# Optimization experiments

Measured on AMD Instinct MI355X. Metric: run time of the kernel, lower is better.

Reference implementation:

```python
import jax, jax.numpy as jnp
import numpy as np

HIDDEN = 2048
HEADS = 16
HEAD_DIM = HIDDEN // HEADS

def setup_inputs() -> dict:
    key = jax.random.key(0)
    ks = jax.random.split(key, 9)
    B, S = 1, 4096
    scale = 1.0 / np.sqrt(HIDDEN)
    x = jax.random.normal(ks[0], (B, S, HIDDEN), dtype=jnp.float32)
    Wq = jax.random.normal(ks[1], (HIDDEN, HIDDEN), dtype=jnp.float32) * scale
    Wk = jax.random.normal(ks[2], (HIDDEN, HIDDEN), dtype=jnp.float32) * scale
    Wv = jax.random.normal(ks[3], (HIDDEN, HIDDEN), dtype=jnp.float32) * scale
    Wo = jax.random.normal(ks[4], (HIDDEN, HIDDEN), dtype=jnp.float32) * scale
    bq = jax.random.normal(ks[5], (HIDDEN,), dtype=jnp.float32) * 0.01
    bk = jax.random.normal(ks[6], (HIDDEN,), dtype=jnp.float32) * 0.01
    bv = jax.random.normal(ks[7], (HIDDEN,), dtype=jnp.float32) * 0.01
    bo = jax.random.normal(ks[8], (HIDDEN,), dtype=jnp.float32) * 0.01
    return {"x": x, "Wq": Wq, "bq": bq, "Wk": Wk, "bk": bk, "Wv": Wv, "bv": bv, "Wo": Wo, "bo": bo}

def reference(x, Wq, bq, Wk, bk, Wv, bv, Wo, bo):
    B, S, D = x.shape
    H, Hd = HEADS, HEAD_DIM
    # projections (nn.Linear: x @ W^T + b)
    Q = (x @ Wq.T + bq).reshape(B, S, H, Hd).transpose(0, 2, 1, 3)  # [B,H,S,Hd]
    K = (x @ Wk.T + bk).reshape(B, S, H, Hd).transpose(0, 2, 1, 3)
    V = (x @ Wv.T + bv).reshape(B, S, H, Hd).transpose(0, 2, 1, 3)
    scores = jnp.einsum('bhqd,bhkd->bhqk', Q, K) / jnp.sqrt(jnp.float32(Hd))
    attn = jax.nn.softmax(scores, axis=-1)
    out = jnp.einsum('bhqk,bhkd->bhqd', attn, V)  # [B,H,S,Hd]
    out = out.transpose(0, 2, 1, 3).reshape(B, S, D)
    return out @ Wo.T + bo
```

## Files before the change

kernel.cpp:

```cpp
#include <hip/hip_runtime.h>

#define S_LEN  4096
#define DMODEL 2048
#define NHEADS 16
#define HDIM   128

typedef __bf16 bf16x8 __attribute__((ext_vector_type(8)));
typedef __bf16 bf16x2 __attribute__((ext_vector_type(2)));
typedef float  f32x4  __attribute__((ext_vector_type(4)));
typedef float  f32x16 __attribute__((ext_vector_type(16)));

__device__ __forceinline__ unsigned short f2b(float f) {
    unsigned int u = __float_as_uint(f);
    unsigned int r = (u + 0x7fffu + ((u >> 16) & 1u)) >> 16;
    return (unsigned short)r;
}

__device__ __forceinline__ unsigned int pkbf16(float a, float b) {
#if __has_builtin(__builtin_amdgcn_cvt_pk_bf16_f32)
    bf16x2 t = __builtin_amdgcn_cvt_pk_bf16_f32(a, b);
    return *(unsigned int*)&t;
#else
    return (unsigned int)f2b(a) | ((unsigned int)f2b(b) << 16);
#endif
}

__device__ __forceinline__ f32x4 mfma16(bf16x8 a, bf16x8 b, f32x4 c) {
    return __builtin_amdgcn_mfma_f32_16x16x32_bf16(a, b, c, 0, 0, 0);
}

__device__ __forceinline__ f32x16 mfma32(bf16x8 a, bf16x8 b, f32x16 c) {
    return __builtin_amdgcn_mfma_f32_32x32x16_bf16(a, b, c, 0, 0, 0);
}

__device__ __forceinline__ void ldg2lds16(const void* g, void* l) {
    __builtin_amdgcn_global_load_lds(
        (__attribute__((address_space(1))) void*)(void*)g,
        (__attribute__((address_space(3))) void*)l, 16, 0, 0);
}

__global__ __launch_bounds__(256) void cvt_bf16(
    const float* __restrict__ src, unsigned short* __restrict__ dst, int n4)
{
    int i = blockIdx.x * blockDim.x + threadIdx.x;
    if (i < n4) {
        float4 v = ((const float4*)src)[i];
        uint2 h;
        h.x = pkbf16(v.x, v.y); h.y = pkbf16(v.z, v.w);
        ((uint2*)dst)[i] = h;
    }
}

__global__ __launch_bounds__(256) void cvt_bf16_w4(
    const float* __restrict__ w0, const float* __restrict__ w1,
    const float* __restrict__ w2, const float* __restrict__ w3,
    unsigned short* __restrict__ d0, unsigned short* __restrict__ d1,
    unsigned short* __restrict__ d2, unsigned short* __restrict__ d3)
{
    const int z = blockIdx.y;
    const float* src = (z == 0) ? w0 : (z == 1) ? w1 : (z == 2) ? w2 : w3;
    unsigned short* dst = (z == 0) ? d0 : (z == 1) ? d1 : (z == 2) ? d2 : d3;
    int i = blockIdx.x * blockDim.x + threadIdx.x;
    float4 v = ((const float4*)src)[i];
    uint2 h;
    h.x = pkbf16(v.x, v.y); h.y = pkbf16(v.z, v.w);
    ((uint2*)dst)[i] = h;
}

__global__ __launch_bounds__(256, 2) void gemm_qkv(
    const unsigned short* __restrict__ xb,
    const unsigned short* __restrict__ Wqb, const float* __restrict__ bq,
    const unsigned short* __restrict__ Wkb, const float* __restrict__ bk,
    const unsigned short* __restrict__ Wvb, const float* __restrict__ bv,
    unsigned short* __restrict__ Qb, unsigned short* __restrict__ Kb,
    unsigned short* __restrict__ Vb)
{
    const int id  = blockIdx.x + 16 * (blockIdx.y + 32 * blockIdx.z);
    const int swz = (id & 7) * 192 + (id >> 3);
    const int n0 = (swz & 15) * 128;
    const int m0 = ((swz >> 4) & 31) * 128;
    const int z  = swz >> 9;

    const unsigned short* B = (z == 0) ? Wqb : (z == 1) ? Wkb : Wvb;
    const float* bias        = (z == 0) ? bq  : (z == 1) ? bk  : bv;
    unsigned short* C        = (z == 0) ? Qb  : (z == 1) ? Kb  : Vb;
    const float oscale = (z == 0) ? 0.12751743f : 1.0f;

    __shared__ alignas(16) unsigned short As[128 * 32];
    __shared__ alignas(16) unsigned short Bs[128 * 32];

    const int tid = threadIdx.x;
    const int w = tid >> 6, lane = tid & 63, lo = lane & 15, qd = lane >> 4;
    const int wm = (w >> 1) * 64, wn = (w & 1) * 64;
    const int rsel = lane >> 2, csel = (lane & 3) * 8;

    f32x4 acc[4][4] = {};

    for (int k0 = 0; k0 < DMODEL; k0 += 32) {
#pragma unroll
        for (int i = 0; i < 2; i++) {
            int c = w * 2 + i;
            ldg2lds16(&xb[(size_t)(m0 + c * 16 + rsel) * DMODEL + k0 + csel],
                      &As[c * 512]);
            ldg2lds16(&B [(size_t)(n0 + c * 16 + rsel) * DMODEL + k0 + csel],
                      &Bs[c * 512]);
        }
        __syncthreads();

        bf16x8 af[4], bfr[4];
#pragma unroll
        for (int i = 0; i < 4; i++)
            af[i] = *(const bf16x8*)&As[(wm + i * 16 + lo) * 32 + qd * 8];
#pragma unroll
        for (int j = 0; j < 4; j++)
            bfr[j] = *(const bf16x8*)&Bs[(wn + j * 16 + lo) * 32 + qd * 8];
#pragma unroll
        for (int i = 0; i < 4; i++)
#pragma unroll
            for (int j = 0; j < 4; j++)
                acc[i][j] = mfma16(af[i], bfr[j], acc[i][j]);
        __syncthreads();
    }

#pragma unroll
    for (int j = 0; j < 4; j++) {
        int n = n0 + wn + j * 16 + lo;
        float bv_ = bias[n];
#pragma unroll
        for (int i = 0; i < 4; i++) {
#pragma unroll
            for (int r = 0; r < 4; r++) {
                int m = m0 + wm + i * 16 + qd * 4 + r;
                C[(size_t)m * DMODEL + n] = f2b((acc[i][j][r] + bv_) * oscale);
            }
        }
    }
}

__global__ __launch_bounds__(256, 2) void gemm_out(
    const unsigned short* __restrict__ Aatt, const unsigned short* __restrict__ Wob,
    const float* __restrict__ bo, float* __restrict__ out)
{
    const int id  = blockIdx.x + 16 * blockIdx.y;
    const int swz = (id & 7) * 64 + (id >> 3);
    const int n0 = (swz & 15) * 128;
    const int m0 = (swz >> 4) * 128;

    __shared__ alignas(16) unsigned short As[128 * 32];
    __shared__ alignas(16) unsigned short Bs[128 * 32];

    const int tid = threadIdx.x;
    const int w = tid >> 6, lane = tid & 63, lo = lane & 15, qd = lane >> 4;
    const int wm = (w >> 1) * 64, wn = (w & 1) * 64;
    const int rsel = lane >> 2, csel = (lane & 3) * 8;

    f32x4 acc[4][4] = {};

    for (int k0 = 0; k0 < DMODEL; k0 += 32) {
#pragma unroll
        for (int i = 0; i < 2; i++) {
            int c = w * 2 + i;
            ldg2lds16(&Aatt[(size_t)(m0 + c * 16 + rsel) * DMODEL + k0 + csel],
                      &As[c * 512]);
            ldg2lds16(&Wob [(size_t)(n0 + c * 16 + rsel) * DMODEL + k0 + csel],
                      &Bs[c * 512]);
        }
        __syncthreads();

        bf16x8 af[4], bfr[4];
#pragma unroll
        for (int i = 0; i < 4; i++)
            af[i] = *(const bf16x8*)&As[(wm + i * 16 + lo) * 32 + qd * 8];
#pragma unroll
        for (int j = 0; j < 4; j++)
            bfr[j] = *(const bf16x8*)&Bs[(wn + j * 16 + lo) * 32 + qd * 8];
#pragma unroll
        for (int i = 0; i < 4; i++)
#pragma unroll
            for (int j = 0; j < 4; j++)
                acc[i][j] = mfma16(af[i], bfr[j], acc[i][j]);
        __syncthreads();
    }

#pragma unroll
    for (int j = 0; j < 4; j++) {
        int n = n0 + wn + j * 16 + lo;
        float bv_ = bo[n];
#pragma unroll
        for (int i = 0; i < 4; i++) {
#pragma unroll
            for (int r = 0; r < 4; r++) {
                int m = m0 + wm + i * 16 + qd * 4 + r;
                out[(size_t)m * DMODEL + n] = acc[i][j][r] + bv_;
            }
        }
    }
}

__global__ __launch_bounds__(256) void transpose_v(
    const unsigned short* __restrict__ Vb, unsigned short* __restrict__ Vt)
{
    __shared__ unsigned short tile[64 * 67];
    const int s0 = blockIdx.x * 64;
    const int d0 = blockIdx.y * 64;
    const int tid = threadIdx.x;
#pragma unroll
    for (int i = 0; i < 2; i++) {
        int chunk = tid + i * 256;
        int r = chunk >> 3, c8 = (chunk & 7) * 8;
        uint4 v = *(const uint4*)&Vb[(size_t)(s0 + r) * DMODEL + d0 + c8];
        const unsigned short* p = (const unsigned short*)&v;
#pragma unroll
        for (int j = 0; j < 8; j++) tile[r * 67 + c8 + j] = p[j];
    }
    __syncthreads();
#pragma unroll
    for (int i = 0; i < 2; i++) {
        int chunk = tid + i * 256;
        int r = chunk >> 3, c8 = (chunk & 7) * 8;
        unsigned short tmp[8];
#pragma unroll
        for (int j = 0; j < 8; j++) tmp[j] = tile[(c8 + j) * 67 + r];
        *(uint4*)&Vt[(size_t)(d0 + r) * S_LEN + s0 + c8] = *(uint4*)tmp;
    }
}

__global__ __launch_bounds__(256, 2) void attn_kernel(
    const unsigned short* __restrict__ Qb, const unsigned short* __restrict__ Kb,
    const unsigned short* __restrict__ Vt, unsigned short* __restrict__ Ob)
{
    const int id = blockIdx.x;
    const int xcd = id & 7, slot = id >> 3;
    const int h  = (xcd << 1) | (slot >> 6);
    const int q0 = (slot & 63) * 64;

    __shared__ alignas(16) unsigned char smem[66048];
    unsigned short* Ks0  = (unsigned short*)smem;
    unsigned short* Vts0 = (unsigned short*)(smem + 16384);
    unsigned short* Ks1  = (unsigned short*)(smem + 32768);
    unsigned short* Vts1 = (unsigned short*)(smem + 49152);
    float* Of = (float*)smem;
    float* Lf = (float*)(smem + 65536);

    const int tid = threadIdx.x;
    const int w = tid >> 6, lane = tid & 63;
    const int qw = w >> 1, kw = w & 1;
    const int l31 = lane & 31, hi = lane >> 5;
    const int sw7 = l31 & 7;

    bf16x8 qf[8];
    {
        const unsigned short* qrow =
            &Qb[(size_t)(q0 + qw * 32 + l31) * DMODEL + h * HDIM];
#pragma unroll
        for (int sl = 0; sl < 8; sl++)
            qf[sl] = *(const bf16x8*)&qrow[sl * 16 + hi * 8];
    }

    f32x16 o_acc[4] = {};
    float l_run = 0.f;

    const int krow = kw * 32 + l31;

#define STAGE_K(dst_, key0_)                                                  \
    {                                                                         \
        _Pragma("unroll")                                                     \
        for (int i = 0; i < 4; i++) {                                         \
            int r = w * 16 + i * 4 + (lane >> 4);                             \
            int c = (lane & 15) ^ (r & 7);                                    \
            ldg2lds16(&Kb[(size_t)((key0_) + r) * DMODEL + h * HDIM + c * 8], \
                      &(dst_)[(w * 16 + i * 4) * 128]);                       \
        }                                                                     \
    }
#define STAGE_V(dst_, key0_)                                                  \
    {                                                                         \
        _Pragma("unroll")                                                     \
        for (int i = 0; i < 4; i++) {                                         \
            int r = w * 32 + i * 8 + (lane >> 3);                             \
            int c = (lane & 7) ^ (r & 7);                                     \
            ldg2lds16(&Vt[(size_t)(h * HDIM + r) * S_LEN + (key0_) + c * 8],  \
                      &(dst_)[(w * 32 + i * 8) * 64]);                        \
        }                                                                     \
    }

#define ATTN_ITER(KsC, VtsC, KsN, VtsN, kbn)                                  \
    {                                                                         \
        if ((kbn) < S_LEN / 64) {                                             \
            STAGE_K(KsN, (kbn) * 64);                                         \
            STAGE_V(VtsN, (kbn) * 64);                                        \
        }                                                                     \
        f32x16 s = {};                                                        \
        __builtin_amdgcn_s_setprio(1);                                        \
        _Pragma("unroll")                                                     \
        for (int sl = 0; sl < 8; sl++) {                                      \
            bf16x8 kf = *(const bf16x8*)                                      \
                &(KsC)[krow * 128 + (((2 * sl + hi) ^ sw7) * 8)];             \
            s = mfma32(kf, qf[sl], s);                                        \
        }                                                                     \
        __builtin_amdgcn_s_setprio(0);                                        \
        bf16x8 pa0, pa1;                                                      \
        {                                                                     \
            float ls = 0.f;                                                   \
            _Pragma("unroll")                                                 \
            for (int k2 = 0; k2 < 2; k2++) {                                  \
                float e0 = __builtin_amdgcn_exp2f(s[8 * k2 + 0]);             \
                float e1 = __builtin_amdgcn_exp2f(s[8 * k2 + 1]);             \
                float e2 = __builtin_amdgcn_exp2f(s[8 * k2 + 2]);             \
                float e3 = __builtin_amdgcn_exp2f(s[8 * k2 + 3]);             \
                float e4 = __builtin_amdgcn_exp2f(s[8 * k2 + 4]);             \
                float e5 = __builtin_amdgcn_exp2f(s[8 * k2 + 5]);             \
                float e6 = __builtin_amdgcn_exp2f(s[8 * k2 + 6]);             \
                float e7 = __builtin_amdgcn_exp2f(s[8 * k2 + 7]);             \
                ls += ((e0 + e1) + (e2 + e3)) + ((e4 + e5) + (e6 + e7));      \
                unsigned int c0 = pkbf16(e0, e1);                             \
                unsigned int c1 = pkbf16(e2, e3);                             \
                unsigned int c2 = pkbf16(e4, e5);                             \
                unsigned int c3 = pkbf16(e6, e7);                             \
                asm("v_permlane32_swap_b32 %0, %1" : "+v"(c0), "+v"(c2));     \
                asm("v_permlane32_swap_b32 %0, %1" : "+v"(c1), "+v"(c3));     \
                uint4 u; u.x = c0; u.y = c1; u.z = c2; u.w = c3;              \
                if (k2 == 0) pa0 = *(bf16x8*)&u; else pa1 = *(bf16x8*)&u;     \
            }                                                                 \
            l_run += ls;                                                      \
        }                                                                     \
        __builtin_amdgcn_s_setprio(1);                                        \
        _Pragma("unroll")                                                     \
        for (int k2 = 0; k2 < 2; k2++) {                                      \
            const int gch = 4 * kw + 2 * k2 + hi;                             \
            bf16x8 pf = (k2 == 0) ? pa0 : pa1;                                \
            _Pragma("unroll")                                                 \
            for (int dt = 0; dt < 4; dt++) {                                  \
                bf16x8 vf = *(const bf16x8*)                                  \
                    &(VtsC)[(dt * 32 + l31) * 64 + ((gch ^ sw7) * 8)];        \
                o_acc[dt] = mfma32(pf, vf, o_acc[dt]);                        \
            }                                                                 \
        }                                                                     \
        __builtin_amdgcn_s_setprio(0);                                        \
        __syncthreads();                                                      \
    }

    STAGE_K(Ks0, 0);
    STAGE_V(Vts0, 0);
    __syncthreads();

    for (int kb = 0; kb < S_LEN / 64; kb += 2) {
        ATTN_ITER(Ks0, Vts0, Ks1, Vts1, kb + 1);
        ATTN_ITER(Ks1, Vts1, Ks0, Vts0, kb + 2);
    }
#undef ATTN_ITER
#undef STAGE_K
#undef STAGE_V

    float l = l_run + __shfl_xor(l_run, 32);

    if (kw == 1) {
#pragma unroll
        for (int dt = 0; dt < 4; dt++)
#pragma unroll
            for (int r = 0; r < 16; r++) {
                int row = (r & 3) + 8 * (r >> 2) + 4 * hi;
                Of[(qw * 32 + row) * 128 + dt * 32 + l31] = o_acc[dt][r];
            }
    }
    if (hi == 0) Lf[(qw * 2 + kw) * 32 + l31] = l;
    __syncthreads();

    if (kw == 0) {
        float linv[16];
#pragma unroll
        for (int r = 0; r < 16; r++) {
            int row = (r & 3) + 8 * (r >> 2) + 4 * hi;
            linv[r] = 1.0f / (Lf[(qw * 2 + 0) * 32 + row] +
                              Lf[(qw * 2 + 1) * 32 + row]);
        }
#pragma unroll
        for (int dt = 0; dt < 4; dt++)
#pragma unroll
            for (int r = 0; r < 16; r++) {
                int row = (r & 3) + 8 * (r >> 2) + 4 * hi;
                float v = o_acc[dt][r] + Of[(qw * 32 + row) * 128 + dt * 32 + l31];
                Ob[(size_t)(q0 + qw * 32 + row) * DMODEL + h * HDIM + dt * 32 + l31]
                    = f2b(v * linv[r]);
            }
    }
}

extern "C" void kernel_launch(void* const* d_in, const int* in_sizes, int n_in,
                              void* d_out, int out_size, void* d_ws, size_t ws_size,
                              hipStream_t stream)
{
    const float* x  = (const float*)d_in[0];
    const float* Wq = (const float*)d_in[1];
    const float* bq = (const float*)d_in[2];
    const float* Wk = (const float*)d_in[3];
    const float* bk = (const float*)d_in[4];
    const float* Wv = (const float*)d_in[5];
    const float* bv = (const float*)d_in[6];
    const float* Wo = (const float*)d_in[7];
    const float* bo = (const float*)d_in[8];
    float* out = (float*)d_out;

    const size_t N = (size_t)S_LEN * DMODEL;
    const size_t W = (size_t)DMODEL * DMODEL;
    unsigned short* Qb  = (unsigned short*)d_ws;
    unsigned short* Kb  = Qb + N;
    unsigned short* Vb  = Kb + N;
    unsigned short* xbv = Vb + N;
    unsigned short* Wqb = xbv + N;
    unsigned short* Wkb = Wqb + W;
    unsigned short* Wvb = Wkb + W;
    unsigned short* Wob = Wvb + W;
    unsigned short* Vt  = xbv;
    unsigned short* Ob  = Vb;

    cvt_bf16<<<(int)(N / 4 / 256), 256, 0, stream>>>(x, xbv, (int)(N / 4));
    cvt_bf16_w4<<<dim3((unsigned)(W / 4 / 256), 4), 256, 0, stream>>>(
        Wq, Wk, Wv, Wo, Wqb, Wkb, Wvb, Wob);

    gemm_qkv<<<dim3(DMODEL / 128, S_LEN / 128, 3), 256, 0, stream>>>(
        xbv, Wqb, bq, Wkb, bk, Wvb, bv, Qb, Kb, Vb);

    transpose_v<<<dim3(S_LEN / 64, DMODEL / 64), 256, 0, stream>>>(Vb, Vt);

    attn_kernel<<<1024, 256, 0, stream>>>(Qb, Kb, Vt, Ob);

    gemm_out<<<dim3(DMODEL / 128, S_LEN / 128), 256, 0, stream>>>(Ob, Wob, bo, out);
}
```

Baseline: 495.7 us.

## Software-pipeline attention QK^T one tile ahead of softmax·V and merge conversion kernels

The attention loop is restructured so the QK^T scores for the next key block are computed while softmax and P·V run for the current block. K is prefetched one tile ahead and V is staged for the current step, and the QK^T chain is split into two independent accumulators to shorten the MFMA dependency chain. LDS is reordered to fit exactly 64KB, and the two fp32->bf16 conversion launches are fused into one kernel writing a contiguous buffer. This trades extra live registers (two score tiles) for overlap of exp/softmax with matrix work, and removes one kernel launch.

```diff
diff --git a/kernel.cpp b/kernel.cpp
--- a/kernel.cpp
+++ b/kernel.cpp
@@ -39,29 +39,21 @@
         (__attribute__((address_space(3))) void*)l, 16, 0, 0);
 }
 
-__global__ __launch_bounds__(256) void cvt_bf16(
-    const float* __restrict__ src, unsigned short* __restrict__ dst, int n4)
-{
-    int i = blockIdx.x * blockDim.x + threadIdx.x;
-    if (i < n4) {
-        float4 v = ((const float4*)src)[i];
-        uint2 h;
-        h.x = pkbf16(v.x, v.y); h.y = pkbf16(v.z, v.w);
-        ((uint2*)dst)[i] = h;
-    }
-}
-
-__global__ __launch_bounds__(256) void cvt_bf16_w4(
+__global__ __launch_bounds__(256) void cvt_all(
+    const float* __restrict__ x,
     const float* __restrict__ w0, const float* __restrict__ w1,
     const float* __restrict__ w2, const float* __restrict__ w3,
-    unsigned short* __restrict__ d0, unsigned short* __restrict__ d1,
-    unsigned short* __restrict__ d2, unsigned short* __restrict__ d3)
-{
-    const int z = blockIdx.y;
-    const float* src = (z == 0) ? w0 : (z == 1) ? w1 : (z == 2) ? w2 : w3;
-    unsigned short* dst = (z == 0) ? d0 : (z == 1) ? d1 : (z == 2) ? d2 : d3;
-    int i = blockIdx.x * blockDim.x + threadIdx.x;
-    float4 v = ((const float4*)src)[i];
+    unsigned short* __restrict__ dst)
+{
+    int i = blockIdx.x * 256 + threadIdx.x;
+    const float* src; int off;
+    if (i < (1 << 21)) { src = x; off = i; }
+    else {
+        int j = i - (1 << 21);
+        int sel = j >> 20; off = j & ((1 << 20) - 1);
+        src = (sel == 0) ? w0 : (sel == 1) ? w1 : (sel == 2) ? w2 : w3;
+    }
+    float4 v = ((const float4*)src)[off];
     uint2 h;
     h.x = pkbf16(v.x, v.y); h.y = pkbf16(v.z, v.w);
     ((uint2*)dst)[i] = h;
@@ -234,13 +226,13 @@
     const int h  = (xcd << 1) | (slot >> 6);
     const int q0 = (slot & 63) * 64;
 
-    __shared__ alignas(16) unsigned char smem[66048];
+    __shared__ alignas(16) unsigned char smem[65536];
     unsigned short* Ks0  = (unsigned short*)smem;
-    unsigned short* Vts0 = (unsigned short*)(smem + 16384);
-    unsigned short* Ks1  = (unsigned short*)(smem + 32768);
+    unsigned short* Ks1  = (unsigned short*)(smem + 16384);
+    unsigned short* Vts0 = (unsigned short*)(smem + 32768);
     unsigned short* Vts1 = (unsigned short*)(smem + 49152);
     float* Of = (float*)smem;
-    float* Lf = (float*)(smem + 65536);
+    float* Lf = (float*)(smem + 32768);
 
     const int tid = threadIdx.x;
     const int w = tid >> 6, lane = tid & 63;
@@ -283,47 +275,46 @@
         }                                                                     \
     }
 
-#define ATTN_ITER(KsC, VtsC, KsN, VtsN, kbn)                                  \
+#define QKT(KsC, SOUT)                                                        \
     {                                                                         \
-        if ((kbn) < S_LEN / 64) {                                             \
-            STAGE_K(KsN, (kbn) * 64);                                         \
-            STAGE_V(VtsN, (kbn) * 64);                                        \
+        f32x16 sa_ = {}, sb_ = {};                                            \
+        _Pragma("unroll")                                                     \
+        for (int sl = 0; sl < 8; sl += 2) {                                   \
+            bf16x8 kfa = *(const bf16x8*)                                     \
+                &(KsC)[krow * 128 + (((2 * sl + hi) ^ sw7) * 8)];             \
+            bf16x8 kfb = *(const bf16x8*)                                     \
+                &(KsC)[krow * 128 + (((2 * (sl + 1) + hi) ^ sw7) * 8)];       \
+            sa_ = mfma32(kfa, qf[sl], sa_);                                   \
+            sb_ = mfma32(kfb, qf[sl + 1], sb_);                               \
         }                                                                     \
-        f32x16 s = {};                                                        \
-        __builtin_amdgcn_s_setprio(1);                                        \
+        SOUT = sa_ + sb_;                                                     \
+    }
+
+#define SMPV(SIN, VtsP)                                                       \
+    {                                                                         \
+        bf16x8 pa0, pa1;                                                      \
+        float ls = 0.f;                                                       \
         _Pragma("unroll")                                                     \
-        for (int sl = 0; sl < 8; sl++) {                                      \
-            bf16x8 kf = *(const bf16x8*)                                      \
-                &(KsC)[krow * 128 + (((2 * sl + hi) ^ sw7) * 8)];             \
-            s = mfma32(kf, qf[sl], s);                                        \
+        for (int k2 = 0; k2 < 2; k2++) {                                      \
+            float e0 = __builtin_amdgcn_exp2f(SIN[8 * k2 + 0]);               \
+            float e1 = __builtin_amdgcn_exp2f(SIN[8 * k2 + 1]);               \
+            float e2 = __builtin_amdgcn_exp2f(SIN[8 * k2 + 2]);               \
+            float e3 = __builtin_amdgcn_exp2f(SIN[8 * k2 + 3]);               \
+            float e4 = __builtin_amdgcn_exp2f(SIN[8 * k2 + 4]);               \
+            float e5 = __builtin_amdgcn_exp2f(SIN[8 * k2 + 5]);               \
+            float e6 = __builtin_amdgcn_exp2f(SIN[8 * k2 + 6]);               \
+            float e7 = __builtin_amdgcn_exp2f(SIN[8 * k2 + 7]);               \
+            ls += ((e0 + e1) + (e2 + e3)) + ((e4 + e5) + (e6 + e7));          \
+            unsigned int c0 = pkbf16(e0, e1);                                 \
+            unsigned int c1 = pkbf16(e2, e3);                                 \
+            unsigned int c2 = pkbf16(e4, e5);                                 \
+            unsigned int c3 = pkbf16(e6, e7);                                 \
+            asm("v_permlane32_swap_b32 %0, %1" : "+v"(c0), "+v"(c2));         \
+            asm("v_permlane32_swap_b32 %0, %1" : "+v"(c1), "+v"(c3));         \
+            uint4 u; u.x = c0; u.y = c1; u.z = c2; u.w = c3;                  \
+            if (k2 == 0) pa0 = *(bf16x8*)&u; else pa1 = *(bf16x8*)&u;         \
         }                                                                     \
-        __builtin_amdgcn_s_setprio(0);                                        \
-        bf16x8 pa0, pa1;                                                      \
-        {                                                                     \
-            float ls = 0.f;                                                   \
-            _Pragma("unroll")                                                 \
-            for (int k2 = 0; k2 < 2; k2++) {                                  \
-                float e0 = __builtin_amdgcn_exp2f(s[8 * k2 + 0]);             \
-                float e1 = __builtin_amdgcn_exp2f(s[8 * k2 + 1]);             \
-                float e2 = __builtin_amdgcn_exp2f(s[8 * k2 + 2]);             \
-                float e3 = __builtin_amdgcn_exp2f(s[8 * k2 + 3]);             \
-                float e4 = __builtin_amdgcn_exp2f(s[8 * k2 + 4]);             \
-                float e5 = __builtin_amdgcn_exp2f(s[8 * k2 + 5]);             \
-                float e6 = __builtin_amdgcn_exp2f(s[8 * k2 + 6]);             \
-                float e7 = __builtin_amdgcn_exp2f(s[8 * k2 + 7]);             \
-                ls += ((e0 + e1) + (e2 + e3)) + ((e4 + e5) + (e6 + e7));      \
-                unsigned int c0 = pkbf16(e0, e1);                             \
-                unsigned int c1 = pkbf16(e2, e3);                             \
-                unsigned int c2 = pkbf16(e4, e5);                             \
-                unsigned int c3 = pkbf16(e6, e7);                             \
-                asm("v_permlane32_swap_b32 %0, %1" : "+v"(c0), "+v"(c2));     \
-                asm("v_permlane32_swap_b32 %0, %1" : "+v"(c1), "+v"(c3));     \
-                uint4 u; u.x = c0; u.y = c1; u.z = c2; u.w = c3;              \
-                if (k2 == 0) pa0 = *(bf16x8*)&u; else pa1 = *(bf16x8*)&u;     \
-            }                                                                 \
-            l_run += ls;                                                      \
-        }                                                                     \
-        __builtin_amdgcn_s_setprio(1);                                        \
+        l_run += ls;                                                          \
         _Pragma("unroll")                                                     \
         for (int k2 = 0; k2 < 2; k2++) {                                      \
             const int gch = 4 * kw + 2 * k2 + hi;                             \
@@ -331,23 +322,43 @@
             _Pragma("unroll")                                                 \
             for (int dt = 0; dt < 4; dt++) {                                  \
                 bf16x8 vf = *(const bf16x8*)                                  \
-                    &(VtsC)[(dt * 32 + l31) * 64 + ((gch ^ sw7) * 8)];        \
+                    &(VtsP)[(dt * 32 + l31) * 64 + ((gch ^ sw7) * 8)];        \
                 o_acc[dt] = mfma32(pf, vf, o_acc[dt]);                        \
             }                                                                 \
         }                                                                     \
+    }
+
+#define ATTN_STEP(t_, KC, KN, VC, VP, SIN, SOUT)                              \
+    {                                                                         \
+        if ((t_) + 1 < S_LEN / 64) STAGE_K(KN, ((t_) + 1) * 64);              \
+        STAGE_V(VC, (t_) * 64);                                               \
+        __builtin_amdgcn_s_setprio(1);                                        \
+        QKT(KC, SOUT);                                                        \
+        SMPV(SIN, VP);                                                        \
         __builtin_amdgcn_s_setprio(0);                                        \
         __syncthreads();                                                      \
     }
 
+    f32x16 sP, sQ;
+
     STAGE_K(Ks0, 0);
+    __syncthreads();
+    STAGE_K(Ks1, 64);
     STAGE_V(Vts0, 0);
+    QKT(Ks0, sP);
     __syncthreads();
 
-    for (int kb = 0; kb < S_LEN / 64; kb += 2) {
-        ATTN_ITER(Ks0, Vts0, Ks1, Vts1, kb + 1);
-        ATTN_ITER(Ks1, Vts1, Ks0, Vts0, kb + 2);
-    }
-#undef ATTN_ITER
+    for (int t = 1; t < S_LEN / 64 - 1; t += 2) {
+        ATTN_STEP(t,     Ks1, Ks0, Vts1, Vts0, sP, sQ);
+        ATTN_STEP(t + 1, Ks0, Ks1, Vts0, Vts1, sQ, sP);
+    }
+    ATTN_STEP(S_LEN / 64 - 1, Ks1, Ks0, Vts1, Vts0, sP, sQ);
+
+    SMPV(sQ, Vts1);
+
+#undef ATTN_STEP
+#undef SMPV
+#undef QKT
 #undef STAGE_K
 #undef STAGE_V
 
@@ -413,9 +424,7 @@
     unsigned short* Vt  = xbv;
     unsigned short* Ob  = Vb;
 
-    cvt_bf16<<<(int)(N / 4 / 256), 256, 0, stream>>>(x, xbv, (int)(N / 4));
-    cvt_bf16_w4<<<dim3((unsigned)(W / 4 / 256), 4), 256, 0, stream>>>(
-        Wq, Wk, Wv, Wo, Wqb, Wkb, Wvb, Wob);
+    cvt_all<<<24576, 256, 0, stream>>>(x, Wq, Wk, Wv, Wo, xbv);
 
     gemm_qkv<<<dim3(DMODEL / 128, S_LEN / 128, 3), 256, 0, stream>>>(
         xbv, Wqb, bq, Wkb, bk, Wvb, bv, Qb, Kb, Vb);
```

Measured after the change: 483.8 us (median of 2 runs). -2.4%, faster.
